# Kernel tuning notes

Hardware: AMD Instinct MI355X
Metric: run time of the kernel (lower is better)

## Reference

```python
import jax, jax.numpy as jnp
import numpy as np

B, T, D, R = 4, 2048, 1024, 32


def setup_inputs() -> dict:
    key = jax.random.key(0)
    kx, ku = jax.random.split(key)
    x = jax.random.normal(kx, (B, T, D), dtype=jnp.float32)
    # low-rank metric factor; small init so distances are moderate
    U = jax.random.normal(ku, (D, R), dtype=jnp.float32) * 0.05
    return {"x": x, "U": U}


def reference(x, U):
    # g = U @ U.T (PSD low-rank metric).
    # dist_sq[b,t,j] = (x_t - x_j)^T g (x_t - x_j)
    #               = ||U^T x_t||^2 + ||U^T x_j||^2 - 2 (U^T x_t).(U^T x_j)
    # Algebraic expansion of the original O(B*T*T*D) broadcasted diff tensor.
    y = jnp.einsum('btd,dr->btr', x, U)                # [B,T,R]
    n = jnp.sum(y * y, axis=-1)                         # [B,T]
    cross = jnp.einsum('btr,bjr->btj', y, y)            # [B,T,T]
    dist_sq = n[:, :, None] + n[:, None, :] - 2.0 * cross
    attn = jax.nn.softmax(-dist_sq, axis=-1)            # [B,T,T]
    return jnp.einsum('btj,bjd->btd', attn, x)          # [B,T,D]
```

## Files before the change

kernel.cpp:

```cpp
#include <hip/hip_runtime.h>

#define B_ 4
#define T_ 2048
#define D_ 1024
#define R_ 32
#define XP 136

typedef __attribute__((ext_vector_type(8))) short short8;
typedef __attribute__((ext_vector_type(4))) float f32x4;
typedef __attribute__((ext_vector_type(4))) unsigned short us4;
typedef __attribute__((ext_vector_type(8))) unsigned short us8;

__device__ __forceinline__ unsigned short f2bf(float f) {
  union { float f; unsigned u; } v; v.f = f;
  unsigned r = (v.u + 0x7fffu + ((v.u >> 16) & 1u)) >> 16;
  return (unsigned short)r;
}
__device__ __forceinline__ float bf2f(unsigned short h) {
  union { unsigned u; float f; } v; v.u = (unsigned)h << 16;
  return v.f;
}

__global__ __launch_bounds__(256)
void geo_prep(const float* __restrict__ x, const float* __restrict__ U,
              unsigned short* __restrict__ xt, float* __restrict__ ypart) {
  __shared__ unsigned short xs[128 * XP];
  __shared__ unsigned short uts[32 * XP];
  const int bb = blockIdx.y, t0 = blockIdx.x * 128, d0 = blockIdx.z * 128;
  const int tid = threadIdx.x, w = tid >> 6, lane = tid & 63;
  const int m = lane & 15, quad = lane >> 4;

  f32x4 uv[4];
  #pragma unroll
  for (int p = 0; p < 4; p++) {
    const int i4 = p * 256 + tid;
    uv[p] = *(const f32x4*)(U + (size_t)(d0 + (i4 >> 3)) * R_ + (i4 & 7) * 4);
  }
  f32x4 xv[16];
  #pragma unroll
  for (int p = 0; p < 16; p++) {
    const int i4 = p * 256 + tid;
    xv[p] = *(const f32x4*)(x + ((size_t)bb * T_ + t0 + (i4 >> 5)) * D_ + d0 + (i4 & 31) * 4);
  }
  #pragma unroll
  for (int p = 0; p < 4; p++) {
    const int i4 = p * 256 + tid; const int du = i4 >> 3, ru4 = i4 & 7;
    #pragma unroll
    for (int k = 0; k < 4; k++) uts[(ru4 * 4 + k) * XP + du] = f2bf(uv[p][k]);
  }
  #pragma unroll
  for (int p = 0; p < 16; p++) {
    const int i4 = p * 256 + tid; const int r = i4 >> 5, c4 = i4 & 31;
    us4 c;
    c[0] = f2bf(xv[p][0]); c[1] = f2bf(xv[p][1]);
    c[2] = f2bf(xv[p][2]); c[3] = f2bf(xv[p][3]);
    *(us4*)&xs[r * XP + c4 * 4] = c;
  }
  __syncthreads();
  {
    const int d = tid >> 1, th = tid & 1;
    unsigned short* xo = xt + ((size_t)bb * D_ + d0 + d) * T_ + t0 + th * 64;
    #pragma unroll
    for (int i = 0; i < 8; i++) {
      us8 o;
      #pragma unroll
      for (int k = 0; k < 8; k++) o[k] = xs[(th * 64 + i * 8 + k) * XP + d];
      *(us8*)(xo + i * 8) = o;
    }
  }
  f32x4 acc[2][2];
  #pragma unroll
  for (int i = 0; i < 2; i++)
    #pragma unroll
    for (int j = 0; j < 2; j++) acc[i][j] = (f32x4){0.f, 0.f, 0.f, 0.f};
  #pragma unroll
  for (int ks = 0; ks < 4; ks++) {
    const int ko = ks * 32 + quad * 8;
    short8 a0 = *(const short8*)&xs[(w * 32 + m) * XP + ko];
    short8 a1 = *(const short8*)&xs[(w * 32 + 16 + m) * XP + ko];
    short8 b0 = *(const short8*)&uts[m * XP + ko];
    short8 b1 = *(const short8*)&uts[(16 + m) * XP + ko];
    acc[0][0] = __builtin_amdgcn_mfma_f32_16x16x32_bf16(a0, b0, acc[0][0], 0, 0, 0);
    acc[0][1] = __builtin_amdgcn_mfma_f32_16x16x32_bf16(a0, b1, acc[0][1], 0, 0, 0);
    acc[1][0] = __builtin_amdgcn_mfma_f32_16x16x32_bf16(a1, b0, acc[1][0], 0, 0, 0);
    acc[1][1] = __builtin_amdgcn_mfma_f32_16x16x32_bf16(a1, b1, acc[1][1], 0, 0, 0);
  }
  #pragma unroll
  for (int tb = 0; tb < 2; tb++)
    #pragma unroll
    for (int nb = 0; nb < 2; nb++)
      *(f32x4*)(ypart + ((size_t)(blockIdx.z * B_ + bb) * R_ + nb * 16 + m) * T_
                + t0 + w * 32 + tb * 16 + quad * 4) = acc[tb][nb];
}

__global__ __launch_bounds__(256)
void geo_reduce(const float* __restrict__ ypart, unsigned short* __restrict__ ybf,
                float* __restrict__ nsq) {
  __shared__ float ls[32 * 132];
  const int t0 = blockIdx.x * 128, bb = blockIdx.y;
  const int tid = threadIdx.x;
  f32x4 vs[4];
  #pragma unroll
  for (int p = 0; p < 4; p++) vs[p] = (f32x4){0.f, 0.f, 0.f, 0.f};
  for (int s = 0; s < 8; s++) {
    #pragma unroll
    for (int p = 0; p < 4; p++) {
      const int i4 = p * 256 + tid;
      f32x4 v = *(const f32x4*)(ypart + ((size_t)(s * B_ + bb) * R_ + (i4 >> 5)) * T_
                                + t0 + (i4 & 31) * 4);
      #pragma unroll
      for (int k = 0; k < 4; k++) vs[p][k] += v[k];
    }
  }
  #pragma unroll
  for (int p = 0; p < 4; p++) {
    const int i4 = p * 256 + tid;
    *(f32x4*)&ls[(i4 >> 5) * 132 + (i4 & 31) * 4] = vs[p];
  }
  __syncthreads();
  const int t = tid >> 1, rh = tid & 1;
  us8 o0, o1; float part = 0.f;
  #pragma unroll
  for (int k = 0; k < 8; k++) {
    const unsigned short h = f2bf(1.69864446f * ls[(rh * 16 + k) * 132 + t]);
    const float bv = bf2f(h); part += bv * bv; o0[k] = h;
  }
  #pragma unroll
  for (int k = 0; k < 8; k++) {
    const unsigned short h = f2bf(1.69864446f * ls[(rh * 16 + 8 + k) * 132 + t]);
    const float bv = bf2f(h); part += bv * bv; o1[k] = h;
  }
  part += __shfl_xor(part, 1, 64);
  unsigned short* yo = ybf + ((size_t)bb * T_ + t0 + t) * R_ + rh * 16;
  *(us8*)yo = o0;
  *(us8*)(yo + 8) = o1;
  if (rh == 0) nsq[bb * T_ + t0 + t] = 0.5f * part;
}

__global__ __launch_bounds__(256, 2)
void geo_fused(const unsigned short* __restrict__ ybf,
               const float* __restrict__ nsq,
               const unsigned short* __restrict__ xt,
               float* __restrict__ out) {
  __shared__ unsigned short Bs[128 * 128];
  __shared__ float l_s[128];
  const int bz = blockIdx.z, id = blockIdx.x;
  const int d0 = (id & 7) * 128;
  const int t0 = (id >> 3) * 128;
  const int tid = threadIdx.x, w = tid >> 6, lane = tid & 63;
  const int m = lane & 15, quad = lane >> 4;
  const int srow4 = lane >> 4, blk = lane & 15;

  const unsigned short* yb = ybf + (size_t)bz * T_ * R_;
  const float* nq = nsq + bz * T_;
  const unsigned short* Xb = xt + ((size_t)bz * D_ + d0) * T_;

#define STAGE(J0) do {                                                           \
    _Pragma("unroll")                                                            \
    for (int cc = 0; cc < 8; cc++) {                                             \
      const int rbase = w * 32 + cc * 4;                                         \
      const int row = rbase + srow4;                                             \
      const int sw = (blk ^ (row & 7)) * 8;                                      \
      __builtin_amdgcn_global_load_lds(                                          \
        (const __attribute__((address_space(1))) void*)(Xb + (size_t)row * T_ + (J0) + sw), \
        (__attribute__((address_space(3))) void*)(Bs + rbase * 128), 16, 0, 0);  \
    } } while (0)

  short8 at[2]; float nnt[2]; float lsum[2] = {0.f, 0.f};
  #pragma unroll
  for (int tb = 0; tb < 2; tb++) {
    at[tb] = *(const short8*)(yb + (size_t)(t0 + w * 32 + tb * 16 + m) * R_ + quad * 8);
    nnt[tb] = -nq[t0 + w * 32 + tb * 16 + m];
  }

  f32x4 acc[2][8];
  #pragma unroll
  for (int i = 0; i < 2; i++)
    #pragma unroll
    for (int j = 0; j < 8; j++) acc[i][j] = (f32x4){0.f, 0.f, 0.f, 0.f};

  for (int it = 0; it < 16; ++it) {
    const int j0 = it * 128;
    __syncthreads();
    STAGE(j0);
    short8 aj[8]; f32x4 njv[8];
    #pragma unroll
    for (int ja = 0; ja < 8; ja++) {
      const int jr = 32 * (ja >> 1) + 8 * (m >> 2) + (ja & 1) * 4 + (m & 3);
      aj[ja] = *(const short8*)(yb + (size_t)(j0 + jr) * R_ + quad * 8);
      njv[ja] = *(const f32x4*)(nq + j0 + 32 * (ja >> 1) + (ja & 1) * 4 + 8 * quad);
    }
    short8 pfrag[2][4];
    #pragma unroll
    for (int tb = 0; tb < 2; tb++) {
      #pragma unroll
      for (int ja = 0; ja < 8; ja++) {
        f32x4 cin;
        #pragma unroll
        for (int r = 0; r < 4; r++) cin[r] = nnt[tb] - njv[ja][r];
        f32x4 c = __builtin_amdgcn_mfma_f32_16x16x32_bf16(aj[ja], at[tb], cin, 0, 0, 0);
        #pragma unroll
        for (int r = 0; r < 4; r++) {
          const float p = __builtin_amdgcn_exp2f(c[r]);
          lsum[tb] += p;
          pfrag[tb][ja >> 1][(ja & 1) * 4 + r] = (short)f2bf(p);
        }
      }
    }
    __syncthreads();
    #pragma unroll
    for (int kb = 0; kb < 4; kb++) {
      short8 bfr[8];
      #pragma unroll
      for (int nb = 0; nb < 8; nb++)
        bfr[nb] = *(const short8*)&Bs[(nb * 16 + m) * 128 + (((kb * 4 + quad) ^ (m & 7)) * 8)];
      #pragma unroll
      for (int tb = 0; tb < 2; tb++)
        #pragma unroll
        for (int nb = 0; nb < 8; nb++)
          acc[tb][nb] = __builtin_amdgcn_mfma_f32_16x16x32_bf16(pfrag[tb][kb], bfr[nb], acc[tb][nb], 0, 0, 0);
    }
  }
  #pragma unroll
  for (int tb = 0; tb < 2; tb++) {
    lsum[tb] += __shfl_xor(lsum[tb], 16, 64);
    lsum[tb] += __shfl_xor(lsum[tb], 32, 64);
  }
  if (quad == 0) { l_s[w * 32 + m] = lsum[0]; l_s[w * 32 + 16 + m] = lsum[1]; }
  __syncthreads();
  #pragma unroll
  for (int tb = 0; tb < 2; tb++) {
    f32x4 lv = *(const f32x4*)&l_s[w * 32 + tb * 16 + quad * 4];
    f32x4 inv;
    #pragma unroll
    for (int r = 0; r < 4; r++) inv[r] = 1.f / lv[r];
    float* ob = out + ((size_t)bz * T_ + t0 + w * 32 + tb * 16 + quad * 4) * D_ + d0;
    #pragma unroll
    for (int nb = 0; nb < 8; nb++)
      #pragma unroll
      for (int r = 0; r < 4; r++)
        ob[(size_t)r * D_ + nb * 16 + m] = acc[tb][nb][r] * inv[r];
  }
#undef STAGE
}

extern "C" void kernel_launch(void* const* d_in, const int* in_sizes, int n_in,
                              void* d_out, int out_size, void* d_ws, size_t ws_size,
                              hipStream_t stream) {
  const float* x = (const float*)d_in[0];
  const float* U = (const float*)d_in[1];
  float* out = (float*)d_out;

  const size_t xt_b  = (size_t)B_ * D_ * T_ * 2;
  const size_t ybf_b = (size_t)B_ * T_ * R_ * 2;
  const size_t nsq_b = (size_t)B_ * T_ * 4;
  const size_t yp_b  = (size_t)8 * B_ * R_ * T_ * 4;

  char* wp = (char*)d_ws;
  unsigned short* xtp = (unsigned short*)wp;                 wp += xt_b;
  unsigned short* ybf = (unsigned short*)wp;                 wp += ybf_b;
  float* nsq = (float*)wp;                                   wp += nsq_b;
  float* ypart = (float*)wp;                                 wp += yp_b;
  (void)ws_size; (void)in_sizes; (void)n_in; (void)out_size;

  hipLaunchKernelGGL(geo_prep, dim3(T_ / 128, B_, D_ / 128), dim3(256), 0, stream,
                     x, U, xtp, ypart);
  hipLaunchKernelGGL(geo_reduce, dim3(T_ / 128, B_), dim3(256), 0, stream,
                     ypart, ybf, nsq);
  hipLaunchKernelGGL(geo_fused, dim3((T_ / 128) * (D_ / 128), 1, B_), dim3(256), 0, stream,
                     ybf, nsq, xtp, out);
}
```

Measured before the change: 176.3 us.

## Double-buffer X tiles in fused attention loop and shrink reduce tiles

The fused kernel now processes the key dimension in 64-wide chunks with two LDS buffers. The next chunk's global-to-LDS load is issued right after the barrier, and the next chunk's y/norm fragments are register-prefetched, so both overlap with the current MFMA work. It also drops one barrier per iteration and keeps the row sums as vector accumulators. The reduce kernel uses 32-row tiles, launching four times as many blocks. The cost is more loop iterations, higher register pressure from the prefetch buffers, and a prefetch that wraps around to index 0 on the final iteration.

```diff
diff --git a/kernel.cpp b/kernel.cpp
--- a/kernel.cpp
+++ b/kernel.cpp
@@ -96,45 +96,33 @@
 __global__ __launch_bounds__(256)
 void geo_reduce(const float* __restrict__ ypart, unsigned short* __restrict__ ybf,
                 float* __restrict__ nsq) {
-  __shared__ float ls[32 * 132];
-  const int t0 = blockIdx.x * 128, bb = blockIdx.y;
+  __shared__ float ls[32][36];
+  const int t0 = blockIdx.x * 32, bb = blockIdx.y;
   const int tid = threadIdx.x;
-  f32x4 vs[4];
-  #pragma unroll
-  for (int p = 0; p < 4; p++) vs[p] = (f32x4){0.f, 0.f, 0.f, 0.f};
-  for (int s = 0; s < 8; s++) {
-    #pragma unroll
-    for (int p = 0; p < 4; p++) {
-      const int i4 = p * 256 + tid;
-      f32x4 v = *(const f32x4*)(ypart + ((size_t)(s * B_ + bb) * R_ + (i4 >> 5)) * T_
-                                + t0 + (i4 & 31) * 4);
+  {
+    const int r = tid >> 3, t4 = (tid & 7) * 4;
+    f32x4 v = {0.f, 0.f, 0.f, 0.f};
+    #pragma unroll
+    for (int s = 0; s < 8; s++) {
+      f32x4 p = *(const f32x4*)(ypart + ((size_t)(s * B_ + bb) * R_ + r) * T_ + t0 + t4);
       #pragma unroll
-      for (int k = 0; k < 4; k++) vs[p][k] += v[k];
+      for (int k = 0; k < 4; k++) v[k] += p[k];
     }
-  }
-  #pragma unroll
-  for (int p = 0; p < 4; p++) {
-    const int i4 = p * 256 + tid;
-    *(f32x4*)&ls[(i4 >> 5) * 132 + (i4 & 31) * 4] = vs[p];
+    *(f32x4*)&ls[r][t4] = v;
   }
   __syncthreads();
-  const int t = tid >> 1, rh = tid & 1;
-  us8 o0, o1; float part = 0.f;
-  #pragma unroll
-  for (int k = 0; k < 8; k++) {
-    const unsigned short h = f2bf(1.69864446f * ls[(rh * 16 + k) * 132 + t]);
-    const float bv = bf2f(h); part += bv * bv; o0[k] = h;
-  }
-  #pragma unroll
-  for (int k = 0; k < 8; k++) {
-    const unsigned short h = f2bf(1.69864446f * ls[(rh * 16 + 8 + k) * 132 + t]);
-    const float bv = bf2f(h); part += bv * bv; o1[k] = h;
-  }
+  const int t = tid >> 3, r4 = (tid & 7) * 4;
+  us4 pk; float part = 0.f;
+  #pragma unroll
+  for (int k = 0; k < 4; k++) {
+    const unsigned short h = f2bf(1.69864446f * ls[r4 + k][t]);
+    const float bv = bf2f(h); part += bv * bv; pk[k] = h;
+  }
+  *(us4*)(ybf + ((size_t)bb * T_ + t0 + t) * R_ + r4) = pk;
   part += __shfl_xor(part, 1, 64);
-  unsigned short* yo = ybf + ((size_t)bb * T_ + t0 + t) * R_ + rh * 16;
-  *(us8*)yo = o0;
-  *(us8*)(yo + 8) = o1;
-  if (rh == 0) nsq[bb * T_ + t0 + t] = 0.5f * part;
+  part += __shfl_xor(part, 2, 64);
+  part += __shfl_xor(part, 4, 64);
+  if ((tid & 7) == 0) nsq[bb * T_ + t0 + t] = 0.5f * part;
 }
 
 __global__ __launch_bounds__(256, 2)
@@ -142,35 +130,77 @@
                const float* __restrict__ nsq,
                const unsigned short* __restrict__ xt,
                float* __restrict__ out) {
-  __shared__ unsigned short Bs[128 * 128];
+  __shared__ unsigned short Bs[2][128 * 64];
   __shared__ float l_s[128];
   const int bz = blockIdx.z, id = blockIdx.x;
   const int d0 = (id & 7) * 128;
   const int t0 = (id >> 3) * 128;
   const int tid = threadIdx.x, w = tid >> 6, lane = tid & 63;
   const int m = lane & 15, quad = lane >> 4;
-  const int srow4 = lane >> 4, blk = lane & 15;
+  const int srow = lane >> 3, sslot = lane & 7;
 
   const unsigned short* yb = ybf + (size_t)bz * T_ * R_;
   const float* nq = nsq + bz * T_;
   const unsigned short* Xb = xt + ((size_t)bz * D_ + d0) * T_;
 
-#define STAGE(J0) do {                                                           \
-    _Pragma("unroll")                                                            \
-    for (int cc = 0; cc < 8; cc++) {                                             \
-      const int rbase = w * 32 + cc * 4;                                         \
-      const int row = rbase + srow4;                                             \
-      const int sw = (blk ^ (row & 7)) * 8;                                      \
+#define STAGE(J0, BUF) do {                                                      \
+    _Pragma("unroll")                                                            \
+    for (int cc = 0; cc < 4; cc++) {                                             \
+      const int rbase = w * 32 + cc * 8;                                         \
+      const int row = rbase + srow;                                              \
+      const int sw = (sslot ^ (row & 7)) * 8;                                    \
       __builtin_amdgcn_global_load_lds(                                          \
         (const __attribute__((address_space(1))) void*)(Xb + (size_t)row * T_ + (J0) + sw), \
-        (__attribute__((address_space(3))) void*)(Bs + rbase * 128), 16, 0, 0);  \
+        (__attribute__((address_space(3))) void*)(&Bs[BUF][rbase * 64]), 16, 0, 0); \
     } } while (0)
 
-  short8 at[2]; float nnt[2]; float lsum[2] = {0.f, 0.f};
+#define BODY(IT, AJC, NJC, AJN, NJN, BUFC, BUFN) do {                            \
+    const int j0b = (IT) * 64;                                                   \
+    const int jn0 = (((IT) + 1) & 31) * 64;                                      \
+    _Pragma("unroll")                                                            \
+    for (int ja = 0; ja < 4; ja++) {                                             \
+      const int jr = 32 * (ja >> 1) + 8 * (m >> 2) + (ja & 1) * 4 + (m & 3);     \
+      AJN[ja] = *(const short8*)(yb + (size_t)(jn0 + jr) * R_ + quad * 8);       \
+      NJN[ja] = *(const f32x4*)(nq + jn0 + 32 * (ja >> 1) + (ja & 1) * 4 + 8 * quad); \
+    }                                                                            \
+    short8 pfrag[2][2];                                                          \
+    _Pragma("unroll")                                                            \
+    for (int tb = 0; tb < 2; tb++) {                                             \
+      _Pragma("unroll")                                                          \
+      for (int ja = 0; ja < 4; ja++) {                                           \
+        f32x4 cin;                                                               \
+        _Pragma("unroll")                                                        \
+        for (int r = 0; r < 4; r++) cin[r] = nnt[tb] - NJC[ja][r];               \
+        f32x4 c = __builtin_amdgcn_mfma_f32_16x16x32_bf16(AJC[ja], at[tb], cin, 0, 0, 0); \
+        _Pragma("unroll")                                                        \
+        for (int r = 0; r < 4; r++) {                                            \
+          const float p = __builtin_amdgcn_exp2f(c[r]);                          \
+          lsum4[tb][r] += p;                                                     \
+          pfrag[tb][ja >> 1][(ja & 1) * 4 + r] = (short)f2bf(p);                 \
+        }                                                                        \
+      }                                                                          \
+    }                                                                            \
+    __syncthreads();                    \
+    if ((IT) + 1 < 32) STAGE(j0b + 64, BUFN);                                    \
+    _Pragma("unroll")                                                            \
+    for (int kb = 0; kb < 2; kb++) {                                             \
+      short8 bfr[8];                                                             \
+      _Pragma("unroll")                                                          \
+      for (int nb = 0; nb < 8; nb++)                                             \
+        bfr[nb] = *(const short8*)&Bs[BUFC][(nb * 16 + m) * 64 + (((kb * 4 + quad) ^ (m & 7)) * 8)]; \
+      _Pragma("unroll")                                                          \
+      for (int tb = 0; tb < 2; tb++)                                             \
+        _Pragma("unroll")                                                        \
+        for (int nb = 0; nb < 8; nb++)                                           \
+          acc[tb][nb] = __builtin_amdgcn_mfma_f32_16x16x32_bf16(pfrag[tb][kb], bfr[nb], acc[tb][nb], 0, 0, 0); \
+    } } while (0)
+
+  short8 at[2]; float nnt[2]; f32x4 lsum4[2];
   #pragma unroll
   for (int tb = 0; tb < 2; tb++) {
     at[tb] = *(const short8*)(yb + (size_t)(t0 + w * 32 + tb * 16 + m) * R_ + quad * 8);
     nnt[tb] = -nq[t0 + w * 32 + tb * 16 + m];
+    lsum4[tb] = (f32x4){0.f, 0.f, 0.f, 0.f};
   }
 
   f32x4 acc[2][8];
@@ -179,50 +209,25 @@
     #pragma unroll
     for (int j = 0; j < 8; j++) acc[i][j] = (f32x4){0.f, 0.f, 0.f, 0.f};
 
-  for (int it = 0; it < 16; ++it) {
-    const int j0 = it * 128;
-    __syncthreads();
-    STAGE(j0);
-    short8 aj[8]; f32x4 njv[8];
-    #pragma unroll
-    for (int ja = 0; ja < 8; ja++) {
-      const int jr = 32 * (ja >> 1) + 8 * (m >> 2) + (ja & 1) * 4 + (m & 3);
-      aj[ja] = *(const short8*)(yb + (size_t)(j0 + jr) * R_ + quad * 8);
-      njv[ja] = *(const f32x4*)(nq + j0 + 32 * (ja >> 1) + (ja & 1) * 4 + 8 * quad);
-    }
-    short8 pfrag[2][4];
-    #pragma unroll
-    for (int tb = 0; tb < 2; tb++) {
-      #pragma unroll
-      for (int ja = 0; ja < 8; ja++) {
-        f32x4 cin;
-        #pragma unroll
-        for (int r = 0; r < 4; r++) cin[r] = nnt[tb] - njv[ja][r];
-        f32x4 c = __builtin_amdgcn_mfma_f32_16x16x32_bf16(aj[ja], at[tb], cin, 0, 0, 0);
-        #pragma unroll
-        for (int r = 0; r < 4; r++) {
-          const float p = __builtin_amdgcn_exp2f(c[r]);
-          lsum[tb] += p;
-          pfrag[tb][ja >> 1][(ja & 1) * 4 + r] = (short)f2bf(p);
-        }
-      }
-    }
-    __syncthreads();
-    #pragma unroll
-    for (int kb = 0; kb < 4; kb++) {
-      short8 bfr[8];
-      #pragma unroll
-      for (int nb = 0; nb < 8; nb++)
-        bfr[nb] = *(const short8*)&Bs[(nb * 16 + m) * 128 + (((kb * 4 + quad) ^ (m & 7)) * 8)];
-      #pragma unroll
-      for (int tb = 0; tb < 2; tb++)
-        #pragma unroll
-        for (int nb = 0; nb < 8; nb++)
-          acc[tb][nb] = __builtin_amdgcn_mfma_f32_16x16x32_bf16(pfrag[tb][kb], bfr[nb], acc[tb][nb], 0, 0, 0);
-    }
-  }
+  short8 ajA[4], ajB[4]; f32x4 njA[4], njB[4];
+  #pragma unroll
+  for (int ja = 0; ja < 4; ja++) {
+    const int jr = 32 * (ja >> 1) + 8 * (m >> 2) + (ja & 1) * 4 + (m & 3);
+    ajA[ja] = *(const short8*)(yb + (size_t)jr * R_ + quad * 8);
+    njA[ja] = *(const f32x4*)(nq + 32 * (ja >> 1) + (ja & 1) * 4 + 8 * quad);
+  }
+  STAGE(0, 0);
+
+  for (int it2 = 0; it2 < 16; it2++) {
+    const int it0 = it2 * 2;
+    BODY(it0,     ajA, njA, ajB, njB, 0, 1);
+    BODY(it0 + 1, ajB, njB, ajA, njA, 1, 0);
+  }
+
+  float lsum[2];
   #pragma unroll
   for (int tb = 0; tb < 2; tb++) {
+    lsum[tb] = lsum4[tb][0] + lsum4[tb][1] + lsum4[tb][2] + lsum4[tb][3];
     lsum[tb] += __shfl_xor(lsum[tb], 16, 64);
     lsum[tb] += __shfl_xor(lsum[tb], 32, 64);
   }
@@ -241,6 +246,7 @@
       for (int r = 0; r < 4; r++)
         ob[(size_t)r * D_ + nb * 16 + m] = acc[tb][nb][r] * inv[r];
   }
+#undef BODY
 #undef STAGE
 }
 
@@ -265,7 +271,7 @@
 
   hipLaunchKernelGGL(geo_prep, dim3(T_ / 128, B_, D_ / 128), dim3(256), 0, stream,
                      x, U, xtp, ypart);
-  hipLaunchKernelGGL(geo_reduce, dim3(T_ / 128, B_), dim3(256), 0, stream,
+  hipLaunchKernelGGL(geo_reduce, dim3(T_ / 32, B_), dim3(256), 0, stream,
                      ypart, ybf, nsq);
   hipLaunchKernelGGL(geo_fused, dim3((T_ / 128) * (D_ / 128), 1, B_), dim3(256), 0, stream,
                      ybf, nsq, xtp, out);
```

New measurement: 175.4 us. About the same (-0.5%).
